# Performance work log

Hardware: AMD Instinct MI355X
Metric: run time of the kernel (lower is better)

The kernel has to match this reference:

```python
import jax, jax.numpy as jnp
import numpy as np

B, EMBED, H, W = 16, 256, 64, 64
HEADS, POINTS = 8, 4  # mmcv MultiScaleDeformableAttention defaults, num_levels=1


def make_pe(d, h, w):
    # LoFTR-style PositionEncodingSine: pe[0::4]=sin(x*div), pe[1::4]=cos(x*div),
    # pe[2::4]=sin(y*div), pe[3::4]=cos(y*div); x,y are 1-based cumsum positions.
    y = jnp.broadcast_to(jnp.arange(1, h + 1, dtype=jnp.float32)[:, None], (h, w))
    x = jnp.broadcast_to(jnp.arange(1, w + 1, dtype=jnp.float32)[None, :], (h, w))
    div = jnp.exp(jnp.arange(0, d // 2, 2, dtype=jnp.float32) * (-np.log(10000.0) / (d // 2)))
    div = div[:, None, None]  # (d//4,1,1)
    pe = jnp.stack([jnp.sin(x * div), jnp.cos(x * div), jnp.sin(y * div), jnp.cos(y * div)], axis=1)
    return pe.reshape(d, h, w)[None]  # (1,d,h,w)


def reference_points(h, w):
    # Faithful to original: meshgrid(linspace(0,1,W), linspace(0,1,H), indexing='ij'),
    # stack (col, row), flatten -> (W*H, 2)
    gx, gy = jnp.meshgrid(jnp.linspace(0.0, 1.0, w), jnp.linspace(0.0, 1.0, h), indexing='ij')
    return jnp.stack([gy, gx], -1).reshape(-1, 2)


def reference(query, value, W_off, b_off, W_attn, b_attn, W_val, b_val, W_out, b_out):
    Bq, C, h, w = query.shape
    N = h * w
    d = C // HEADS
    pe = make_pe(C, h, w)
    q = query + pe  # query += self.pe(query)
    q_flat = q.reshape(Bq, C, N).transpose(0, 2, 1)      # (B,N,C)
    v_flat = value.reshape(Bq, C, N).transpose(0, 2, 1)  # (B,N,C)
    # value projection, split heads: (B,heads,N,d) -- spatial index n = y*w + x
    v = (v_flat @ W_val.T + b_val).reshape(Bq, N, HEADS, d).transpose(0, 2, 1, 3)
    off = (q_flat @ W_off.T + b_off).reshape(Bq, N, HEADS, POINTS, 2)
    attn = jax.nn.softmax((q_flat @ W_attn.T + b_attn).reshape(Bq, N, HEADS, POINTS), axis=-1)
    ref = reference_points(h, w)                          # (N,2)
    normalizer = jnp.array([w, h], jnp.float32)           # (W, H) per mmcv
    loc = ref[None, :, None, None, :] + off / normalizer  # (B,N,heads,P,2) in [0,1]
    grid = 2.0 * loc - 1.0                                # grid_sample coords, align_corners=False
    sx = grid[..., 0].transpose(0, 2, 1, 3).reshape(Bq, HEADS, N * POINTS)
    sy = grid[..., 1].transpose(0, 2, 1, 3).reshape(Bq, HEADS, N * POINTS)
    ix = (sx + 1.0) * w * 0.5 - 0.5
    iy = (sy + 1.0) * h * 0.5 - 0.5
    x0f = jnp.floor(ix); y0f = jnp.floor(iy)
    wx = ix - x0f; wy = iy - y0f
    x0 = x0f.astype(jnp.int32); y0 = y0f.astype(jnp.int32)

    def gather(yi, xi):
        # zero padding outside the image
        valid = (xi >= 0) & (xi < w) & (yi >= 0) & (yi < h)
        idx = jnp.clip(yi, 0, h - 1) * w + jnp.clip(xi, 0, w - 1)  # (B,heads,M)
        g = jnp.take_along_axis(v, idx[..., None], axis=2)          # (B,heads,M,d)
        return g * valid[..., None]

    samp = (((1 - wx) * (1 - wy))[..., None] * gather(y0, x0)
            + (wx * (1 - wy))[..., None] * gather(y0, x0 + 1)
            + ((1 - wx) * wy)[..., None] * gather(y0 + 1, x0)
            + (wx * wy)[..., None] * gather(y0 + 1, x0 + 1))        # (B,heads,N*P,d)
    samp = samp.reshape(Bq, HEADS, N, POINTS, d)
    attn_t = attn.transpose(0, 2, 1, 3)                             # (B,heads,N,P)
    out = jnp.einsum('bhnp,bhnpd->bnhd', attn_t, samp).reshape(Bq, N, C)
    out = out @ W_out.T + b_out + q_flat  # mmcv internal identity residual (dropout in eval = id)
    out = out.transpose(0, 2, 1).reshape(Bq, C, h, w)
    return out + q  # outer residual: output + query (query already has pe added)


def setup_inputs():
    key = jax.random.key(0)
    ks = jax.random.split(key, 8)
    s = 0.02
    return {
        'query': jax.random.normal(ks[0], (B, EMBED, H, W), jnp.float32),
        'value': jax.random.normal(ks[1], (B, EMBED, H, W), jnp.float32),
        'W_off': jax.random.normal(ks[2], (HEADS * POINTS * 2, EMBED), jnp.float32) * s,
        'b_off': jax.random.normal(ks[3], (HEADS * POINTS * 2,), jnp.float32) * 2.0,
        'W_attn': jax.random.normal(ks[4], (HEADS * POINTS, EMBED), jnp.float32) * s,
        'b_attn': jnp.zeros((HEADS * POINTS,), jnp.float32),
        'W_val': jax.random.normal(ks[5], (EMBED, EMBED), jnp.float32) * s,
        'b_val': jnp.zeros((EMBED,), jnp.float32),
        'W_out': jax.random.normal(ks[6], (EMBED, EMBED), jnp.float32) * s,
        'b_out': jnp.zeros((EMBED,), jnp.float32),
    }
```

## Files before the change

kernel.cpp:

```cpp
#include <hip/hip_runtime.h>
#include <hip/hip_bf16.h>

typedef __bf16 bf16;
typedef bf16 bf16x8 __attribute__((ext_vector_type(8)));
typedef bf16 bf16x4 __attribute__((ext_vector_type(4)));
typedef float f32x4 __attribute__((ext_vector_type(4)));

#define CB 16
#define CC 256
#define CH 64
#define CW 64
#define CN 4096
#define NHEADS 8
#define NPOINTS 4
#define HDIM 32
#define TBP 132

#define MFMA16(a, b, c) __builtin_amdgcn_mfma_f32_16x16x32_bf16(a, b, c, 0, 0, 0)

__device__ __forceinline__ void gload16(const void* g, void* l) {
    __builtin_amdgcn_global_load_lds((const __attribute__((address_space(1))) void*)g,
                                     (__attribute__((address_space(3))) void*)l, 16, 0, 0);
}

__global__ __launch_bounds__(256) void pe_pack(float* __restrict__ pe,
                                               const float* __restrict__ Wv,
                                               const float* __restrict__ Woff,
                                               const float* __restrict__ Wattn,
                                               const float* __restrict__ Wout,
                                               bf16* __restrict__ Wv_bf,
                                               bf16* __restrict__ W96_bf,
                                               bf16* __restrict__ Wout_bf) {
    int idx = blockIdx.x * 256 + threadIdx.x;
    if (idx < CC * CN) {
        int c = idx >> 12, n = idx & (CN - 1);
        int r = n >> 6, x = n & 63;
        int i = c >> 2, t = c & 3;
        float div = __expf(-logf(10000.0f) * (float)i / 64.0f);
        float arg = ((t < 2) ? (float)(x + 1) : (float)(r + 1)) * div;
        pe[idx] = (t & 1) ? cosf(arg) : sinf(arg);
    }
    if (idx < CC * CC) {
        Wv_bf[idx] = (bf16)Wv[idx];
        Wout_bf[idx] = (bf16)Wout[idx];
    }
    if (idx < 96 * CC) {
        W96_bf[idx] = (bf16)((idx < 64 * CC) ? Woff[idx] : Wattn[idx - 64 * CC]);
    }
}

__global__ __launch_bounds__(512) void vproj_f(const float* __restrict__ value,
                                               const bf16* __restrict__ Wv,
                                               const float* __restrict__ bv,
                                               bf16* __restrict__ v_s) {
    __shared__ __align__(16) char smem[17408];
    float* T = (float*)smem;
    const int TP = 66;

    int tid = threadIdx.x, lane = tid & 63, wave = tid >> 6;
    int wm = wave >> 1, wn = wave & 1, g = lane >> 4, lr = lane & 15;
    int n0 = blockIdx.x * 64, b = blockIdx.z;
    int nl = tid & 63, kg = tid >> 6;
    const float* src = value + (size_t)b * CC * CN + n0 + nl;

    float v[8];
#pragma unroll
    for (int p = 0; p < 8; ++p) v[p] = src[(size_t)(kg * 8 + p) * CN];

    f32x4 acc[4][2] = {};
    for (int t = 0; t < 4; ++t) {
        bf16x8 o;
#pragma unroll
        for (int p = 0; p < 8; ++p) o[p] = (bf16)v[p];
        *(bf16x8*)(smem + (t & 1) * 8192 + nl * 128 + ((kg ^ (nl & 7)) * 16)) = o;
        __syncthreads();
        if (t < 3) {
#pragma unroll
            for (int p = 0; p < 8; ++p) v[p] = src[(size_t)((t + 1) * 64 + kg * 8 + p) * CN];
        }
#pragma unroll
        for (int ks = 0; ks < 2; ++ks) {
            bf16x8 af[4], bfr[2];
#pragma unroll
            for (int mf = 0; mf < 4; ++mf)
                af[mf] = *(const bf16x8*)&Wv[(size_t)(wm * 64 + mf * 16 + lr) * CC + t * 64 + ks * 32 + g * 8];
#pragma unroll
            for (int nf = 0; nf < 2; ++nf) {
                int row = wn * 32 + nf * 16 + lr;
                bfr[nf] = *(const bf16x8*)(smem + (t & 1) * 8192 + row * 128 + (((ks * 4 + g) ^ (row & 7)) * 16));
            }
#pragma unroll
            for (int mf = 0; mf < 4; ++mf)
#pragma unroll
                for (int nf = 0; nf < 2; ++nf)
                    acc[mf][nf] = MFMA16(af[mf], bfr[nf], acc[mf][nf]);
        }
    }

    int q = tid & 3, n_l = (tid >> 2) & 63, hh = tid >> 8;
#pragma unroll
    for (int pass = 0; pass < 4; ++pass) {
        __syncthreads();
        if (wm == pass) {
#pragma unroll
            for (int mf = 0; mf < 4; ++mf)
#pragma unroll
                for (int nf = 0; nf < 2; ++nf)
#pragma unroll
                    for (int i = 0; i < 4; ++i)
                        T[(mf * 16 + g * 4 + i) * TP + wn * 32 + nf * 16 + lr] = acc[mf][nf][i];
        }
        __syncthreads();
        int head = pass * 2 + hh;
        bf16x8 o;
#pragma unroll
        for (int u = 0; u < 8; ++u)
            o[u] = (bf16)(T[(hh * 32 + q * 8 + u) * TP + n_l] + bv[pass * 64 + hh * 32 + q * 8 + u]);
        *(bf16x8*)&v_s[(((size_t)b * NHEADS + head) * CN + n0 + n_l) * HDIM + q * 8] = o;
    }
}

__global__ __launch_bounds__(256, 4) void offattn_sample(const float* __restrict__ query,
                                                         const float* __restrict__ pe,
                                                         const bf16* __restrict__ W96,
                                                         const float* __restrict__ boff,
                                                         const float* __restrict__ battn,
                                                         const bf16* __restrict__ v_s,
                                                         bf16* __restrict__ s) {
    __shared__ __align__(16) char smem[33792];
    float* ot = (float*)smem;
    unsigned* tbl = (unsigned*)smem;

    int tid = threadIdx.x, lane = tid & 63, wave = tid >> 6;
    int wm = wave >> 1, wn = wave & 1, g = lane >> 4, lr = lane & 15;
    int id = blockIdx.x;
    int xcd = id & 7, local = id >> 3;
    int b = xcd * 2 + (local >> 6);
    int nt = local & 63;
    int n0 = nt * 64;
    int nl = tid & 63, kg = tid >> 6;
    const float* qs = query + (size_t)b * CC * CN + n0 + nl;
    const float* ps = pe + n0 + nl;

    float v[16];
#pragma unroll
    for (int p = 0; p < 16; ++p) {
        size_t off = (size_t)(kg * 16 + p) * CN;
        v[p] = __builtin_nontemporal_load(&qs[off]) + ps[off];
    }
    asm volatile("" ::: "memory");

    f32x4 acc[3][2] = {};
    for (int t = 0; t < 4; ++t) {
#pragma unroll
        for (int half = 0; half < 2; ++half) {
            bf16x8 o;
#pragma unroll
            for (int p = 0; p < 8; ++p) o[p] = (bf16)v[half * 8 + p];
            int slot = (kg * 2 + half) ^ (nl & 7);
            *(bf16x8*)(smem + (t & 1) * 8192 + nl * 128 + slot * 16) = o;
        }
        __syncthreads();
        if (t < 3) {
#pragma unroll
            for (int p = 0; p < 16; ++p) {
                size_t off = (size_t)((t + 1) * 64 + kg * 16 + p) * CN;
                v[p] = __builtin_nontemporal_load(&qs[off]) + ps[off];
            }
            asm volatile("" ::: "memory");
        }
#pragma unroll
        for (int ks = 0; ks < 2; ++ks) {
            bf16x8 af[3], bfr[2];
#pragma unroll
            for (int mf = 0; mf < 3; ++mf)
                af[mf] = *(const bf16x8*)&W96[(size_t)(wm * 48 + mf * 16 + lr) * CC + t * 64 + ks * 32 + g * 8];
#pragma unroll
            for (int nf = 0; nf < 2; ++nf) {
                int row = wn * 32 + nf * 16 + lr;
                bfr[nf] = *(const bf16x8*)(smem + (t & 1) * 8192 + row * 128 + (((ks * 4 + g) ^ (row & 7)) * 16));
            }
#pragma unroll
            for (int mf = 0; mf < 3; ++mf)
#pragma unroll
                for (int nf = 0; nf < 2; ++nf)
                    acc[mf][nf] = MFMA16(af[mf], bfr[nf], acc[mf][nf]);
        }
    }
    __syncthreads();

#pragma unroll
    for (int mf = 0; mf < 3; ++mf) {
#pragma unroll
        for (int i = 0; i < 4; ++i) {
            int j = wm * 48 + mf * 16 + g * 4 + i;
            float bias = (j < 64) ? boff[j] : battn[j - 64];
#pragma unroll
            for (int nf = 0; nf < 2; ++nf) {
                int col = wn * 32 + nf * 16 + lr;
                ot[j * 65 + col] = acc[mf][nf][i] + bias;
            }
        }
    }
    __syncthreads();

    unsigned pk[2][16];
#pragma unroll
    for (int it = 0; it < 2; ++it) {
        int item = it * 256 + tid;
        int inl = item & 63, h = item >> 6;
        float lg0 = ot[(64 + h * 4 + 0) * 65 + inl];
        float lg1 = ot[(64 + h * 4 + 1) * 65 + inl];
        float lg2 = ot[(64 + h * 4 + 2) * 65 + inl];
        float lg3 = ot[(64 + h * 4 + 3) * 65 + inl];
        float m = fmaxf(fmaxf(lg0, lg1), fmaxf(lg2, lg3));
        float e0 = __expf(lg0 - m), e1 = __expf(lg1 - m);
        float e2 = __expf(lg2 - m), e3 = __expf(lg3 - m);
        float inv = 1.0f / (e0 + e1 + e2 + e3);
        float ep[4] = {e0, e1, e2, e3};
#pragma unroll
        for (int p = 0; p < NPOINTS; ++p) {
            float off0 = ot[(h * 8 + p * 2 + 0) * 65 + inl];
            float off1 = ot[(h * 8 + p * 2 + 1) * 65 + inl];
            float ix = (float)inl * (64.0f / 63.0f) + off0 - 0.5f;
            float iy = (float)nt * (64.0f / 63.0f) + off1 - 0.5f;
            float x0f = floorf(ix), y0f = floorf(iy);
            float wx = ix - x0f, wy = iy - y0f;
            int x0 = (int)x0f, y0 = (int)y0f;
            int x1 = x0 + 1, y1 = y0 + 1;
            float vx0 = (x0 >= 0 && x0 < CW) ? 1.f : 0.f;
            float vx1 = (x1 >= 0 && x1 < CW) ? 1.f : 0.f;
            float vy0 = (y0 >= 0 && y0 < CH) ? 1.f : 0.f;
            float vy1 = (y1 >= 0 && y1 < CH) ? 1.f : 0.f;
            int x0c = min(max(x0, 0), CW - 1), x1c = min(max(x1, 0), CW - 1);
            int y0c = min(max(y0, 0), CH - 1), y1c = min(max(y1, 0), CH - 1);
            float a = ep[p] * inv;
            float w00 = a * (1.f - wx) * (1.f - wy) * vx0 * vy0;
            float w01 = a * wx * (1.f - wy) * vx1 * vy0;
            float w10 = a * (1.f - wx) * wy * vx0 * vy1;
            float w11 = a * wx * wy * vx1 * vy1;
            unsigned c00 = (unsigned)(y0c * CW + x0c), c01 = (unsigned)(y0c * CW + x1c);
            unsigned c10 = (unsigned)(y1c * CW + x0c), c11 = (unsigned)(y1c * CW + x1c);
            pk[it][p * 4 + 0] = ((unsigned)__builtin_bit_cast(unsigned short, (_Float16)w00) << 16) | c00;
            pk[it][p * 4 + 1] = ((unsigned)__builtin_bit_cast(unsigned short, (_Float16)w01) << 16) | c01;
            pk[it][p * 4 + 2] = ((unsigned)__builtin_bit_cast(unsigned short, (_Float16)w10) << 16) | c10;
            pk[it][p * 4 + 3] = ((unsigned)__builtin_bit_cast(unsigned short, (_Float16)w11) << 16) | c11;
        }
    }
    __syncthreads();
#pragma unroll
    for (int it = 0; it < 2; ++it) {
        int item = it * 256 + tid;
        int inl = item & 63, h = item >> 6;
        uint4* dst = (uint4*)(tbl + inl * TBP + h * 16);
#pragma unroll
        for (int j = 0; j < 4; ++j) {
            uint4 w4;
            w4.x = pk[it][j * 4 + 0]; w4.y = pk[it][j * 4 + 1];
            w4.z = pk[it][j * 4 + 2]; w4.w = pk[it][j * 4 + 3];
            dst[j] = w4;
        }
    }
    __syncthreads();

    int q = tid & 3, h2 = (tid >> 2) & 7, ng = tid >> 5;
    const bf16* vb = v_s + (((size_t)b * NHEADS + h2) * CN) * HDIM + q * 8;
#pragma unroll
    for (int iter = 0; iter < 8; ++iter) {
        int snl = iter * 8 + ng;
        const uint4* tb4 = (const uint4*)(tbl + snl * TBP + h2 * 16);
        unsigned ue[16];
#pragma unroll
        for (int j = 0; j < 4; ++j) {
            uint4 t4 = tb4[j];
            ue[j * 4 + 0] = t4.x; ue[j * 4 + 1] = t4.y;
            ue[j * 4 + 2] = t4.z; ue[j * 4 + 3] = t4.w;
        }
        asm volatile("" ::: "memory");
        bf16x8 gr[16];
#pragma unroll
        for (int e = 0; e < 16; ++e)
            gr[e] = *(const bf16x8*)&vb[(int)(ue[e] & 0xFFFu) * HDIM];
        asm volatile("" ::: "memory");
        float a0 = 0.f, a1 = 0.f, a2 = 0.f, a3 = 0.f;
        float a4 = 0.f, a5 = 0.f, a6 = 0.f, a7 = 0.f;
#pragma unroll
        for (int e = 0; e < 16; ++e) {
            float w = (float)__builtin_bit_cast(_Float16, (unsigned short)(ue[e] >> 16));
            a0 += w * (float)gr[e][0]; a1 += w * (float)gr[e][1];
            a2 += w * (float)gr[e][2]; a3 += w * (float)gr[e][3];
            a4 += w * (float)gr[e][4]; a5 += w * (float)gr[e][5];
            a6 += w * (float)gr[e][6]; a7 += w * (float)gr[e][7];
        }
        bf16x8 o;
        o[0] = (bf16)a0; o[1] = (bf16)a1; o[2] = (bf16)a2; o[3] = (bf16)a3;
        o[4] = (bf16)a4; o[5] = (bf16)a5; o[6] = (bf16)a6; o[7] = (bf16)a7;
        *(bf16x8*)&s[((size_t)b * CN + n0 + snl) * CC + h2 * 32 + q * 8] = o;
    }
}

__global__ __launch_bounds__(256) void outproj_v7(const bf16* __restrict__ s_t,
                                                  const bf16* __restrict__ Wout,
                                                  const float* __restrict__ bout,
                                                  const float* __restrict__ query,
                                                  const float* __restrict__ pe,
                                                  float* __restrict__ out) {
    __shared__ __align__(16) char smem[33792];
    float* T = (float*)smem;
    const int TP = 132;

    int tid = threadIdx.x, lane = tid & 63, wave = tid >> 6;
    int wm = wave >> 1, wn = wave & 1, g = lane >> 4, lr = lane & 15;
    int id = blockIdx.x;
    int swz = (id & 7) * 128 + (id >> 3);
    int n0 = (swz & 31) * 128, c0 = ((swz >> 5) & 1) * 128, b = swz >> 6;
    const bf16* sb = s_t + ((size_t)b * CN + n0) * CC;

    f32x4 acc[4][4] = {};
    for (int t = 0; t < 4; ++t) {
        if (t) __syncthreads();
#pragma unroll
        for (int j = 0; j < 4; ++j) {
            int blkrow = (wave * 4 + j) * 8;
            int row = blkrow + (lane >> 3);
            int chunk = (lane & 7) ^ (row & 7);
            const bf16* gA = sb + (size_t)row * CC + t * 64 + chunk * 8;
            const bf16* gB = Wout + (size_t)(c0 + row) * CC + t * 64 + chunk * 8;
            gload16(gA, smem + (wave * 4 + j) * 1024);
            gload16(gB, smem + 16384 + (wave * 4 + j) * 1024);
        }
        __syncthreads();
#pragma unroll
        for (int ks = 0; ks < 2; ++ks) {
            bf16x8 af[4], bfr[4];
#pragma unroll
            for (int mf = 0; mf < 4; ++mf) {
                int row = wm * 64 + mf * 16 + lr;
                af[mf] = *(const bf16x8*)(smem + row * 128 + (((ks * 4 + g) ^ (row & 7)) * 16));
            }
#pragma unroll
            for (int nf = 0; nf < 4; ++nf) {
                int row = wn * 64 + nf * 16 + lr;
                bfr[nf] = *(const bf16x8*)(smem + 16384 + row * 128 + (((ks * 4 + g) ^ (row & 7)) * 16));
            }
#pragma unroll
            for (int mf = 0; mf < 4; ++mf)
#pragma unroll
                for (int nf = 0; nf < 4; ++nf)
                    acc[mf][nf] = MFMA16(af[mf], bfr[nf], acc[mf][nf]);
        }
    }
    __syncthreads();

    int lr5 = tid & 31, rq = tid >> 5;
#pragma unroll
    for (int ch = 0; ch < 2; ++ch) {
        if (wn == ch) {
#pragma unroll
            for (int mf = 0; mf < 4; ++mf)
#pragma unroll
                for (int nf = 0; nf < 4; ++nf) {
                    int cl = nf * 16 + lr;
                    int nl = wm * 64 + mf * 16 + g * 4;
                    *(f32x4*)&T[cl * TP + nl] = acc[mf][nf];
                }
        }
        __syncthreads();
#pragma unroll
        for (int pass = 0; pass < 8; ++pass) {
            int cl = pass * 8 + rq;
            int c = c0 + ch * 64 + cl;
            int n = n0 + lr5 * 4;
            f32x4 v = *(const f32x4*)&T[cl * TP + lr5 * 4];
            size_t base = ((size_t)b * CC + c) * CN + n;
            f32x4 q4 = *(const f32x4*)&query[base];
            f32x4 p4 = *(const f32x4*)&pe[(size_t)c * CN + n];
            float bias = bout[c];
#pragma unroll
            for (int j = 0; j < 4; ++j) v[j] = v[j] + bias + 2.0f * (q4[j] + p4[j]);
            *(f32x4*)&out[base] = v;
        }
        __syncthreads();
    }
}

extern "C" void kernel_launch(void* const* d_in, const int* in_sizes, int n_in,
                              void* d_out, int out_size, void* d_ws, size_t ws_size,
                              hipStream_t stream) {
    const float* query = (const float*)d_in[0];
    const float* value = (const float*)d_in[1];
    const float* W_off = (const float*)d_in[2];
    const float* b_off = (const float*)d_in[3];
    const float* W_attn = (const float*)d_in[4];
    const float* b_attn = (const float*)d_in[5];
    const float* W_val = (const float*)d_in[6];
    const float* b_val = (const float*)d_in[7];
    const float* W_out = (const float*)d_in[8];
    const float* b_out = (const float*)d_in[9];
    float* out = (float*)d_out;

    char* p = (char*)d_ws;
    float* pe = (float*)p;            p += (size_t)CC * CN * 4;
    bf16* Wv_bf = (bf16*)p;           p += (size_t)CC * CC * 2;
    bf16* Wout_bf = (bf16*)p;         p += (size_t)CC * CC * 2;
    bf16* W96_bf = (bf16*)p;          p += (size_t)96 * CC * 2 + 256;
    bf16* v_s = (bf16*)p;             p += (size_t)CB * NHEADS * CN * HDIM * 2;
    bf16* s_t = (bf16*)p;             p += (size_t)CB * CN * CC * 2;

    pe_pack<<<dim3((CC * CN + 255) / 256), dim3(256), 0, stream>>>(pe, W_val, W_off, W_attn,
                                                                   W_out, Wv_bf, W96_bf, Wout_bf);
    vproj_f<<<dim3(CN / 64, 1, CB), dim3(512), 0, stream>>>(value, Wv_bf, b_val, v_s);
    offattn_sample<<<dim3(1024), dim3(256), 0, stream>>>(query, pe, W96_bf,
                                                         b_off, b_attn, v_s, s_t);
    outproj_v7<<<dim3(1024), dim3(256), 0, stream>>>(s_t, Wout_bf, b_out, query, pe, out);
}
```

Measured before the change: 137.5 us.

## Split value projection across output-channel halves with smaller blocks

```diff
diff --git a/kernel.cpp b/kernel.cpp
--- a/kernel.cpp
+++ b/kernel.cpp
@@ -49,7 +49,7 @@
     }
 }
 
-__global__ __launch_bounds__(512) void vproj_f(const float* __restrict__ value,
+__global__ __launch_bounds__(256) void vproj_g(const float* __restrict__ value,
                                                const bf16* __restrict__ Wv,
                                                const float* __restrict__ bv,
                                                bf16* __restrict__ v_s) {
@@ -59,31 +59,36 @@
 
     int tid = threadIdx.x, lane = tid & 63, wave = tid >> 6;
     int wm = wave >> 1, wn = wave & 1, g = lane >> 4, lr = lane & 15;
-    int n0 = blockIdx.x * 64, b = blockIdx.z;
+    int n0 = blockIdx.x * 64, m0 = blockIdx.y * 128, b = blockIdx.z;
     int nl = tid & 63, kg = tid >> 6;
     const float* src = value + (size_t)b * CC * CN + n0 + nl;
 
-    float v[8];
-#pragma unroll
-    for (int p = 0; p < 8; ++p) v[p] = src[(size_t)(kg * 8 + p) * CN];
+    float v[16];
+#pragma unroll
+    for (int p = 0; p < 16; ++p) v[p] = src[(size_t)(kg * 16 + p) * CN];
 
     f32x4 acc[4][2] = {};
     for (int t = 0; t < 4; ++t) {
-        bf16x8 o;
-#pragma unroll
-        for (int p = 0; p < 8; ++p) o[p] = (bf16)v[p];
-        *(bf16x8*)(smem + (t & 1) * 8192 + nl * 128 + ((kg ^ (nl & 7)) * 16)) = o;
+#pragma unroll
+        for (int half = 0; half < 2; ++half) {
+            bf16x8 o;
+#pragma unroll
+            for (int p = 0; p < 8; ++p) o[p] = (bf16)v[half * 8 + p];
+            int slot = (kg * 2 + half) ^ (nl & 7);
+            *(bf16x8*)(smem + (t & 1) * 8192 + nl * 128 + slot * 16) = o;
+        }
         __syncthreads();
         if (t < 3) {
 #pragma unroll
-            for (int p = 0; p < 8; ++p) v[p] = src[(size_t)((t + 1) * 64 + kg * 8 + p) * CN];
+            for (int p = 0; p < 16; ++p)
+                v[p] = src[(size_t)((t + 1) * 64 + kg * 16 + p) * CN];
         }
 #pragma unroll
         for (int ks = 0; ks < 2; ++ks) {
             bf16x8 af[4], bfr[2];
 #pragma unroll
             for (int mf = 0; mf < 4; ++mf)
-                af[mf] = *(const bf16x8*)&Wv[(size_t)(wm * 64 + mf * 16 + lr) * CC + t * 64 + ks * 32 + g * 8];
+                af[mf] = *(const bf16x8*)&Wv[(size_t)(m0 + wm * 64 + mf * 16 + lr) * CC + t * 64 + ks * 32 + g * 8];
 #pragma unroll
             for (int nf = 0; nf < 2; ++nf) {
                 int row = wn * 32 + nf * 16 + lr;
@@ -97,9 +102,8 @@
         }
     }
 
-    int q = tid & 3, n_l = (tid >> 2) & 63, hh = tid >> 8;
-#pragma unroll
-    for (int pass = 0; pass < 4; ++pass) {
+#pragma unroll
+    for (int pass = 0; pass < 2; ++pass) {
         __syncthreads();
         if (wm == pass) {
 #pragma unroll
@@ -111,12 +115,18 @@
                         T[(mf * 16 + g * 4 + i) * TP + wn * 32 + nf * 16 + lr] = acc[mf][nf][i];
         }
         __syncthreads();
-        int head = pass * 2 + hh;
-        bf16x8 o;
-#pragma unroll
-        for (int u = 0; u < 8; ++u)
-            o[u] = (bf16)(T[(hh * 32 + q * 8 + u) * TP + n_l] + bv[pass * 64 + hh * 32 + q * 8 + u]);
-        *(bf16x8*)&v_s[(((size_t)b * NHEADS + head) * CN + n0 + n_l) * HDIM + q * 8] = o;
+#pragma unroll
+        for (int it = 0; it < 2; ++it) {
+            int item = it * 256 + tid;
+            int qg = item & 7, n_l = item >> 3;
+            int cg = m0 + pass * 64 + qg * 8;
+            int head = cg >> 5, dd0 = cg & 31;
+            bf16x8 o;
+#pragma unroll
+            for (int u = 0; u < 8; ++u)
+                o[u] = (bf16)(T[(qg * 8 + u) * TP + n_l] + bv[cg + u]);
+            *(bf16x8*)&v_s[(((size_t)b * NHEADS + head) * CN + n0 + n_l) * HDIM + dd0] = o;
+        }
     }
 }
 
@@ -409,7 +419,7 @@
 
     pe_pack<<<dim3((CC * CN + 255) / 256), dim3(256), 0, stream>>>(pe, W_val, W_off, W_attn,
                                                                    W_out, Wv_bf, W96_bf, Wout_bf);
-    vproj_f<<<dim3(CN / 64, 1, CB), dim3(512), 0, stream>>>(value, Wv_bf, b_val, v_s);
+    vproj_g<<<dim3(CN / 64, 2, CB), dim3(256), 0, stream>>>(value, Wv_bf, b_val, v_s);
     offattn_sample<<<dim3(1024), dim3(256), 0, stream>>>(query, pe, W96_bf,
                                                          b_off, b_attn, v_s, s_t);
     outproj_v7<<<dim3(1024), dim3(256), 0, stream>>>(s_t, Wout_bf, b_out, query, pe, out);
```

Measured after the change: 134.9 us (median of 2 runs). No clear change (-1.9%).
